# Performance work log

Hardware: AMD Instinct MI355X
Metric: run time of the kernel (lower is better)

The kernel has to match this reference:

```python
import jax, jax.numpy as jnp
import numpy as np

# Static problem sizes (uniform T/taus make the ragged edge list static).
B, N, F, T, TAU, S = 8, 384, 64, 192, 192, 5
SINK_SHIFT = T                    # min sink index == T (sinks are the new nodes)
N_SINK, N_SOURCE = TAU, T + TAU - 1


def _edge_indices():
    # tril_indices(T+tau, offset=-1), keep sink >= T  (window=None)
    r, c = np.tril_indices(T + TAU, k=-1)
    m = r >= T
    r, c = r[m], c[m]
    e = r.shape[0]
    batch = np.repeat(np.arange(B), e)
    return (jnp.asarray(batch, jnp.int32),
            jnp.asarray(np.tile(r, B), jnp.int32),
            jnp.asarray(np.tile(c, B), jnp.int32))


def setup_inputs() -> dict:
    key = jax.random.key(0)
    ks = jax.random.split(key, 6)
    batch_idx, sink_idx, source_idx = _edge_indices()
    s1, s2 = 1.0 / np.sqrt(2 * F), 1.0 / np.sqrt(F)
    return {
        "nodes": jax.random.normal(ks[0], (B, N, F), jnp.float32),
        "w1": jax.random.uniform(ks[1], (2 * F, F), jnp.float32, -s1, s1),
        "b1": jnp.zeros((F,), jnp.float32),
        "g1": jnp.ones((F,), jnp.float32),
        "be1": jnp.zeros((F,), jnp.float32),
        "w2": jax.random.uniform(ks[2], (F, F), jnp.float32, -s2, s2),
        "b2": jnp.zeros((F,), jnp.float32),
        "g2": jnp.ones((F,), jnp.float32),
        "be2": jnp.zeros((F,), jnp.float32),
        "w3": jax.random.uniform(ks[3], (F, 1), jnp.float32, -s2, s2),
        "b3": jnp.zeros((1,), jnp.float32),
        "gumbel": jax.random.gumbel(ks[4], (S, B, N_SINK, N_SOURCE), jnp.float32),
        "batch_idx": batch_idx,
        "sink_idx": sink_idx,
        "source_idx": source_idx,
    }


def _ln(x, g, b):
    mu = x.mean(-1, keepdims=True)
    v = ((x - mu) ** 2).mean(-1, keepdims=True)
    return (x - mu) * jax.lax.rsqrt(v + 1e-5) * g + b


def reference(nodes, w1, b1, g1, be1, w2, b2, g2, be2, w3, b3,
              gumbel, batch_idx, sink_idx, source_idx):
    # gather sink/source node pairs: [E, 2F]
    sink = nodes[batch_idx, sink_idx]
    src = nodes[batch_idx, source_idx]
    x = jnp.concatenate([sink, src], axis=-1)
    # edge MLP -> per-edge logit
    h = _ln(jax.nn.relu(x @ w1 + b1), g1, be1)
    h = _ln(jax.nn.relu(h @ w2 + b2), g2, be2)
    logits = (h @ w3 + b3)[:, 0]                     # [E]
    # dense-padded grid filled with finfo.min (as in torch)
    neg = jnp.finfo(jnp.float32).min
    gs = jnp.full((B, N_SINK, N_SOURCE), neg, jnp.float32)
    gs = gs.at[batch_idx, sink_idx - SINK_SHIFT, source_idx].set(logits)
    # hard gumbel-softmax over source dim, S independent samples
    y_soft = jax.nn.softmax(gs[None] + gumbel, axis=-1)      # [S,B,192,383]
    y_hard = jax.nn.one_hot(jnp.argmax(y_soft, -1), N_SOURCE, dtype=y_soft.dtype)
    y = y_soft + jax.lax.stop_gradient(y_hard - y_soft)
    e = y.sum(0)
    # straight-through binarize: forward (e>0), backward identity
    e = e + jax.lax.stop_gradient((e > 0).astype(e.dtype) - e)
    valid = e[batch_idx, sink_idx - SINK_SHIFT, source_idx]
    vals = jnp.where(valid > 0, valid, 0.0)
    # dense equivalent of the sparse COO adjacency (B, N, N)
    return jnp.zeros((B, N, N), jnp.float32).at[batch_idx, sink_idx, source_idx].set(vals)
```

## Files before the change

kernel.cpp:

```cpp
#include <hip/hip_runtime.h>
#include <math.h>
#include <stdint.h>

#define BB 8
#define NN 384
#define FF 64
#define TT 192
#define NSRC 383
#define NSINK 192
#define SS 5
#define NEDGE 441600
#define BN (BB * NN)
#define TILE_E 256
#define NBLKE (NEDGE / TILE_E)
#define OUTV ((BB * NN * NN) / 4)

typedef _Float16 half8 __attribute__((ext_vector_type(8)));
typedef __fp16 fp16x2 __attribute__((ext_vector_type(2)));
typedef float floatx4 __attribute__((ext_vector_type(4)));

static __device__ __forceinline__ void split_f16(float x, uint16_t& h, uint16_t& l) {
  const _Float16 hh = (_Float16)x;
  const float hb = (float)hh;
  const _Float16 ll = (_Float16)((x - hb) * 512.f);
  h = __builtin_bit_cast(uint16_t, hh);
  l = __builtin_bit_cast(uint16_t, ll);
}

static __device__ __forceinline__ void split_pair(float x0, float x1,
                                                  uint32_t& hi, uint32_t& lo) {
  const fp16x2 h = __builtin_amdgcn_cvt_pkrtz(x0, x1);
  const float hb0 = (float)h.x, hb1 = (float)h.y;
  const fp16x2 l = __builtin_amdgcn_cvt_pkrtz((x0 - hb0) * 512.f, (x1 - hb1) * 512.f);
  hi = __builtin_bit_cast(uint32_t, h);
  lo = __builtin_bit_cast(uint32_t, l);
}

__global__ __launch_bounds__(64) void prep_all(
    const float* __restrict__ nodes, const float* __restrict__ w1,
    const float* __restrict__ b1,
    const float* __restrict__ w2, const float* __restrict__ b2,
    const float* __restrict__ g1, const float* __restrict__ be1,
    const float* __restrict__ g2, const float* __restrict__ be2,
    const float* __restrict__ w3, const float* __restrict__ b3,
    float* __restrict__ A, float* __restrict__ Bv,
    unsigned short* __restrict__ Whg, unsigned short* __restrict__ Wlg,
    float* __restrict__ wcol, float* __restrict__ cb,
    float* __restrict__ gw, float* __restrict__ cwsgw) {
  const int blk = blockIdx.x;
  const int k = threadIdx.x;
  if (blk < BN / 4) {
    const int bn0 = blk * 4;
    __shared__ float nd[4][FF];
#pragma unroll
    for (int i = 0; i < 4; ++i) nd[i][k] = nodes[(bn0 + i) * FF + k];
    __syncthreads();
    const float bk = b1[k];
    float a0 = bk, a1 = bk, a2 = bk, a3 = bk;
    float q0 = 0.f, q1 = 0.f, q2 = 0.f, q3 = 0.f;
#pragma unroll 8
    for (int f = 0; f < FF; ++f) {
      const float wt = w1[f * FF + k];
      const float wb = w1[(FF + f) * FF + k];
      const float n0 = nd[0][f], n1 = nd[1][f], n2 = nd[2][f], n3 = nd[3][f];
      a0 = fmaf(n0, wt, a0); a1 = fmaf(n1, wt, a1);
      a2 = fmaf(n2, wt, a2); a3 = fmaf(n3, wt, a3);
      q0 = fmaf(n0, wb, q0); q1 = fmaf(n1, wb, q1);
      q2 = fmaf(n2, wb, q2); q3 = fmaf(n3, wb, q3);
    }
    A[(bn0 + 0) * FF + k] = a0;  Bv[(bn0 + 0) * FF + k] = q0;
    A[(bn0 + 1) * FF + k] = a1;  Bv[(bn0 + 1) * FF + k] = q1;
    A[(bn0 + 2) * FF + k] = a2;  Bv[(bn0 + 2) * FF + k] = q2;
    A[(bn0 + 3) * FF + k] = a3;  Bv[(bn0 + 3) * FF + k] = q3;
  } else {
    const int j = k;
    const int jt = j >> 4, m = j & 15;
    float cbj = b2[j];
    float wc = 0.f;
    for (int kk = 0; kk < FF; ++kk) {
      const float wraw = w2[kk * FF + j];
      const float w = g1[kk] * wraw;
      wc += w;
      cbj = fmaf(be1[kk], wraw, cbj);
      uint16_t hu, lu;
      split_f16(w, hu, lu);
      const int kc = kk >> 5, qq = (kk >> 3) & 3, jj = kk & 7;
      const int idx = (((jt * 2 + kc) * 4 + qq) * 16 + m) * 8 + jj;
      Whg[idx] = hu;
      Wlg[idx] = lu;
    }
    wcol[j] = wc;
    cb[j] = cbj;
    const float gwj = g2[j] * w3[j];
    gw[j] = gwj;
    __shared__ float sA[FF], sB[FF];
    sA[j] = gwj;
    sB[j] = be2[j] * w3[j];
    __syncthreads();
    if (j == 0) {
      float a = 0.f, bq = 0.f;
      for (int i = 0; i < FF; ++i) { a += sA[i]; bq += sB[i]; }
      cwsgw[0] = b3[0] + bq;
      cwsgw[1] = a;
    }
  }
}

__global__ __launch_bounds__(256, 2) void edge_mlp(
    const float* __restrict__ A, const float* __restrict__ Bv,
    const unsigned short* __restrict__ Whg, const unsigned short* __restrict__ Wlg,
    const float* __restrict__ wcolg, const float* __restrict__ cbg,
    const float* __restrict__ gwg, const float* __restrict__ cwsgw,
    const int* __restrict__ bidx, const int* __restrict__ ridx,
    const int* __restrict__ cidx, float* __restrict__ L,
    float4* __restrict__ outv) {
  __shared__ __align__(16) unsigned short XHs[16384];
  __shared__ __align__(16) unsigned short XLs[16384];

  const int tid = threadIdx.x;
  const int wave = tid >> 6;
  const int lane = tid & 63;
  const int q4 = lane >> 4;
  const int c15 = lane & 15;

  const int gtid = blockIdx.x * 256 + tid;
  if (gtid < OUTV) outv[gtid] = make_float4(0.f, 0.f, 0.f, 0.f);

  half8 whr[4][2], wlr[4][2];
#pragma unroll
  for (int jt = 0; jt < 4; ++jt)
#pragma unroll
    for (int kc = 0; kc < 2; ++kc) {
      const int woff = ((jt * 2 + kc) * 4 + q4) * 128 + c15 * 8;
      whr[jt][kc] = *(const half8*)&Whg[woff];
      wlr[jt][kc] = *(const half8*)&Wlg[woff];
    }

  const int ge = blockIdx.x * TILE_E + tid;
  const int b = bidx[ge], r = ridx[ge], c = cidx[ge];
  const int et_own = lane >> 4, n_own = lane & 15;
  float mu, rstd;
  {
    const float4* pa = (const float4*)(A + (b * NN + r) * FF);
    const float4* pb = (const float4*)(Bv + (b * NN + c) * FF);
    unsigned short* dh = &XHs[wave * 4096 + n_own * 8];
    unsigned short* dl = &XLs[wave * 4096 + n_own * 8];
    float s = 0.f, q = 0.f;
#pragma unroll
    for (int g = 0; g < 8; ++g) {
      const float4 av0 = pa[2 * g], av1 = pa[2 * g + 1];
      const float4 bv0 = pb[2 * g], bv1 = pb[2 * g + 1];
      const float x0 = fmaxf(av0.x + bv0.x, 0.f);
      const float x1 = fmaxf(av0.y + bv0.y, 0.f);
      const float x2 = fmaxf(av0.z + bv0.z, 0.f);
      const float x3 = fmaxf(av0.w + bv0.w, 0.f);
      const float x4 = fmaxf(av1.x + bv1.x, 0.f);
      const float x5 = fmaxf(av1.y + bv1.y, 0.f);
      const float x6 = fmaxf(av1.z + bv1.z, 0.f);
      const float x7 = fmaxf(av1.w + bv1.w, 0.f);
      s += x0 + x1 + x2 + x3 + x4 + x5 + x6 + x7;
      q = fmaf(x0, x0, q); q = fmaf(x1, x1, q);
      q = fmaf(x2, x2, q); q = fmaf(x3, x3, q);
      q = fmaf(x4, x4, q); q = fmaf(x5, x5, q);
      q = fmaf(x6, x6, q); q = fmaf(x7, x7, q);
      int4 hi4, lo4;
      split_pair(x0, x1, *(uint32_t*)&hi4.x, *(uint32_t*)&lo4.x);
      split_pair(x2, x3, *(uint32_t*)&hi4.y, *(uint32_t*)&lo4.y);
      split_pair(x4, x5, *(uint32_t*)&hi4.z, *(uint32_t*)&lo4.z);
      split_pair(x6, x7, *(uint32_t*)&hi4.w, *(uint32_t*)&lo4.w);
      const int choff = ((et_own * 2 + (g >> 2)) * 4 + (g & 3)) * 128;
      *(int4*)(dh + choff) = hi4;
      *(int4*)(dl + choff) = lo4;
    }
    mu = s * (1.f / FF);
    rstd = 1.f / sqrtf(q * (1.f / FF) - mu * mu + 1e-5f);
  }

  __syncthreads();

  floatx4 wc4[4], cb4[4], gw4[4];
#pragma unroll
  for (int jt = 0; jt < 4; ++jt) {
    wc4[jt] = *(const floatx4*)(wcolg + 16 * jt + 4 * q4);
    cb4[jt] = *(const floatx4*)(cbg + 16 * jt + 4 * q4);
    gw4[jt] = *(const floatx4*)(gwg + 16 * jt + 4 * q4);
  }
  const float cw = cwsgw[0], sgw = cwsgw[1];

#pragma unroll
  for (int et = 0; et < 4; ++et) {
    floatx4 acc0[4], acc1[4];
#pragma unroll
    for (int jt = 0; jt < 4; ++jt) {
      acc0[jt] = (floatx4){0.f, 0.f, 0.f, 0.f};
      acc1[jt] = (floatx4){0.f, 0.f, 0.f, 0.f};
    }
#pragma unroll
    for (int kc = 0; kc < 2; ++kc) {
      const int xoff = wave * 4096 + ((et * 2 + kc) * 4 + q4) * 128 + c15 * 8;
      const half8 xh = *(const half8*)&XHs[xoff];
      const half8 xl = *(const half8*)&XLs[xoff];
#pragma unroll
      for (int jt = 0; jt < 4; ++jt) {
        acc0[jt] = __builtin_amdgcn_mfma_f32_16x16x32_f16(whr[jt][kc], xh, acc0[jt], 0, 0, 0);
        acc1[jt] = __builtin_amdgcn_mfma_f32_16x16x32_f16(whr[jt][kc], xl, acc1[jt], 0, 0, 0);
        acc1[jt] = __builtin_amdgcn_mfma_f32_16x16x32_f16(wlr[jt][kc], xh, acc1[jt], 0, 0, 0);
      }
    }
    const int e2 = 16 * et + c15;
    const float mue = __shfl(mu, e2, 64);
    const float rse = __shfl(rstd, e2, 64);
    float s1 = 0.f, s2 = 0.f, s3 = 0.f;
#pragma unroll
    for (int jt = 0; jt < 4; ++jt) {
      const floatx4 t4 = acc0[jt] + acc1[jt] * (1.f / 512.f);
#pragma unroll
      for (int rg = 0; rg < 4; ++rg) {
        const float pre = fmaf(rse, fmaf(-mue, wc4[jt][rg], t4[rg]), cb4[jt][rg]);
        const float tr = fmaxf(pre, 0.f);
        s1 += tr;
        s2 = fmaf(tr, tr, s2);
        s3 = fmaf(tr, gw4[jt][rg], s3);
      }
    }
    s1 += __shfl_xor(s1, 16, 64); s1 += __shfl_xor(s1, 32, 64);
    s2 += __shfl_xor(s2, 16, 64); s2 += __shfl_xor(s2, 32, 64);
    s3 += __shfl_xor(s3, 16, 64); s3 += __shfl_xor(s3, 32, 64);
    const int b2 = __shfl(b, e2, 64);
    const int r2 = __shfl(r, e2, 64);
    const int c2 = __shfl(c, e2, 64);
    if (q4 == 0) {
      const float mu2 = s1 * (1.f / FF);
      const float var2 = s2 * (1.f / FF) - mu2 * mu2;
      const float rstd2 = 1.f / sqrtf(var2 + 1e-5f);
      const float logit = fmaf(rstd2, fmaf(-mu2, sgw, s3), cw);
      L[(b2 * NSINK + (r2 - TT)) * NSRC + c2] = logit;
    }
  }
}

__global__ __launch_bounds__(256) void argmax_scatter(
    const float* __restrict__ L, const float* __restrict__ gum,
    float* __restrict__ out) {
  const int task = blockIdx.x * 4 + (threadIdx.x >> 6);
  const int lane = threadIdx.x & 63;
  const int row = task % NSINK;
  const int sb = task / NSINK;
  const int b = sb & 7;
  const int r = row + TT;

  const float* __restrict__ lrow = L + (b * NSINK + row) * NSRC;
  const float* __restrict__ grow = gum + task * NSRC;

  float bv = -INFINITY;
  int bi = 0;
  for (int c = lane; c < r; c += 64) {
    const float v = lrow[c] + grow[c];
    if (v > bv) { bv = v; bi = c; }
  }
#pragma unroll
  for (int off = 32; off > 0; off >>= 1) {
    const float ov = __shfl_xor(bv, off, 64);
    const int oi = __shfl_xor(bi, off, 64);
    if (ov > bv || (ov == bv && oi < bi)) { bv = ov; bi = oi; }
  }
  if (lane == 0) out[(b * NN + r) * NN + bi] = 1.0f;
}

extern "C" void kernel_launch(void* const* d_in, const int* in_sizes, int n_in,
                              void* d_out, int out_size, void* d_ws, size_t ws_size,
                              hipStream_t stream) {
  const float* nodes = (const float*)d_in[0];
  const float* w1 = (const float*)d_in[1];
  const float* b1 = (const float*)d_in[2];
  const float* g1 = (const float*)d_in[3];
  const float* be1 = (const float*)d_in[4];
  const float* w2 = (const float*)d_in[5];
  const float* b2 = (const float*)d_in[6];
  const float* g2 = (const float*)d_in[7];
  const float* be2 = (const float*)d_in[8];
  const float* w3 = (const float*)d_in[9];
  const float* b3 = (const float*)d_in[10];
  const float* gum = (const float*)d_in[11];
  const int* bidx = (const int*)d_in[12];
  const int* ridx = (const int*)d_in[13];
  const int* cidx = (const int*)d_in[14];
  float* out = (float*)d_out;

  float* ws = (float*)d_ws;
  float* A = ws;
  float* Bv = A + BN * FF;
  unsigned short* Whg = (unsigned short*)(ws + 393216);
  unsigned short* Wlg = Whg + 4096;
  float* wcol = ws + 397312;
  float* cb = wcol + FF;
  float* gw = cb + FF;
  float* cwsgw = gw + FF;
  float* L = ws + 397520;
  (void)ws_size; (void)n_in; (void)in_sizes; (void)out_size;

  hipLaunchKernelGGL(prep_all, dim3(BN / 4 + 1), dim3(64), 0, stream,
                     nodes, w1, b1, w2, b2, g1, be1, g2, be2, w3, b3,
                     A, Bv, Whg, Wlg, wcol, cb, gw, cwsgw);
  hipLaunchKernelGGL(edge_mlp, dim3(NBLKE), dim3(256), 0, stream,
                     A, Bv, Whg, Wlg, wcol, cb, gw, cwsgw, bidx, ridx, cidx, L,
                     (float4*)out);
  hipLaunchKernelGGL(argmax_scatter, dim3((SS * BB * NSINK) / 4), dim3(256), 0, stream,
                     L, gum, out);
}
```

Before: 134.7 us.

## Shrink edge MLP blocks, center inputs before split, drop block barrier

Halves the edge tile and block size to 128 threads with new launch bounds, so LDS per block shrinks and more blocks can be resident. Replaces __syncthreads with a wave barrier, since each wave only reads its own LDS region. Computes the layer-1 mean in a first pass and subtracts it before the f16 hi/lo split, which removes the wcol correction term and its loads. The cost is reading the A and B rows twice per edge.

```diff
diff --git a/kernel.cpp b/kernel.cpp
--- a/kernel.cpp
+++ b/kernel.cpp
@@ -11,7 +11,7 @@
 #define SS 5
 #define NEDGE 441600
 #define BN (BB * NN)
-#define TILE_E 256
+#define TILE_E 128
 #define NBLKE (NEDGE / TILE_E)
 #define OUTV ((BB * NN * NN) / 4)
 
@@ -45,8 +45,7 @@
     const float* __restrict__ w3, const float* __restrict__ b3,
     float* __restrict__ A, float* __restrict__ Bv,
     unsigned short* __restrict__ Whg, unsigned short* __restrict__ Wlg,
-    float* __restrict__ wcol, float* __restrict__ cb,
-    float* __restrict__ gw, float* __restrict__ cwsgw) {
+    float* __restrict__ cb, float* __restrict__ gw, float* __restrict__ cwsgw) {
   const int blk = blockIdx.x;
   const int k = threadIdx.x;
   if (blk < BN / 4) {
@@ -76,11 +75,9 @@
     const int j = k;
     const int jt = j >> 4, m = j & 15;
     float cbj = b2[j];
-    float wc = 0.f;
     for (int kk = 0; kk < FF; ++kk) {
       const float wraw = w2[kk * FF + j];
       const float w = g1[kk] * wraw;
-      wc += w;
       cbj = fmaf(be1[kk], wraw, cbj);
       uint16_t hu, lu;
       split_f16(w, hu, lu);
@@ -89,7 +86,6 @@
       Whg[idx] = hu;
       Wlg[idx] = lu;
     }
-    wcol[j] = wc;
     cb[j] = cbj;
     const float gwj = g2[j] * w3[j];
     gw[j] = gwj;
@@ -106,16 +102,16 @@
   }
 }
 
-__global__ __launch_bounds__(256, 2) void edge_mlp(
+__global__ __launch_bounds__(128, 3) void edge_mlp(
     const float* __restrict__ A, const float* __restrict__ Bv,
     const unsigned short* __restrict__ Whg, const unsigned short* __restrict__ Wlg,
-    const float* __restrict__ wcolg, const float* __restrict__ cbg,
-    const float* __restrict__ gwg, const float* __restrict__ cwsgw,
+    const float* __restrict__ cbg, const float* __restrict__ gwg,
+    const float* __restrict__ cwsgw,
     const int* __restrict__ bidx, const int* __restrict__ ridx,
     const int* __restrict__ cidx, float* __restrict__ L,
     float4* __restrict__ outv) {
-  __shared__ __align__(16) unsigned short XHs[16384];
-  __shared__ __align__(16) unsigned short XLs[16384];
+  __shared__ __align__(16) unsigned short XHs[8192];
+  __shared__ __align__(16) unsigned short XLs[8192];
 
   const int tid = threadIdx.x;
   const int wave = tid >> 6;
@@ -123,46 +119,47 @@
   const int q4 = lane >> 4;
   const int c15 = lane & 15;
 
-  const int gtid = blockIdx.x * 256 + tid;
+  const int gtid = blockIdx.x * 128 + tid;
   if (gtid < OUTV) outv[gtid] = make_float4(0.f, 0.f, 0.f, 0.f);
-
-  half8 whr[4][2], wlr[4][2];
-#pragma unroll
-  for (int jt = 0; jt < 4; ++jt)
-#pragma unroll
-    for (int kc = 0; kc < 2; ++kc) {
-      const int woff = ((jt * 2 + kc) * 4 + q4) * 128 + c15 * 8;
-      whr[jt][kc] = *(const half8*)&Whg[woff];
-      wlr[jt][kc] = *(const half8*)&Wlg[woff];
-    }
 
   const int ge = blockIdx.x * TILE_E + tid;
   const int b = bidx[ge], r = ridx[ge], c = cidx[ge];
   const int et_own = lane >> 4, n_own = lane & 15;
+  const float4* pa = (const float4*)(A + (b * NN + r) * FF);
+  const float4* pb = (const float4*)(Bv + (b * NN + c) * FF);
   float mu, rstd;
   {
-    const float4* pa = (const float4*)(A + (b * NN + r) * FF);
-    const float4* pb = (const float4*)(Bv + (b * NN + c) * FF);
+    float s = 0.f, q = 0.f;
+#pragma unroll
+    for (int i = 0; i < 16; ++i) {
+      const float4 av = pa[i];
+      const float4 bv = pb[i];
+      const float x0 = fmaxf(av.x + bv.x, 0.f);
+      const float x1 = fmaxf(av.y + bv.y, 0.f);
+      const float x2 = fmaxf(av.z + bv.z, 0.f);
+      const float x3 = fmaxf(av.w + bv.w, 0.f);
+      s += x0 + x1 + x2 + x3;
+      q = fmaf(x0, x0, q); q = fmaf(x1, x1, q);
+      q = fmaf(x2, x2, q); q = fmaf(x3, x3, q);
+    }
+    mu = s * (1.f / FF);
+    rstd = 1.f / sqrtf(q * (1.f / FF) - mu * mu + 1e-5f);
+  }
+  {
     unsigned short* dh = &XHs[wave * 4096 + n_own * 8];
     unsigned short* dl = &XLs[wave * 4096 + n_own * 8];
-    float s = 0.f, q = 0.f;
 #pragma unroll
     for (int g = 0; g < 8; ++g) {
       const float4 av0 = pa[2 * g], av1 = pa[2 * g + 1];
       const float4 bv0 = pb[2 * g], bv1 = pb[2 * g + 1];
-      const float x0 = fmaxf(av0.x + bv0.x, 0.f);
-      const float x1 = fmaxf(av0.y + bv0.y, 0.f);
-      const float x2 = fmaxf(av0.z + bv0.z, 0.f);
-      const float x3 = fmaxf(av0.w + bv0.w, 0.f);
-      const float x4 = fmaxf(av1.x + bv1.x, 0.f);
-      const float x5 = fmaxf(av1.y + bv1.y, 0.f);
-      const float x6 = fmaxf(av1.z + bv1.z, 0.f);
-      const float x7 = fmaxf(av1.w + bv1.w, 0.f);
-      s += x0 + x1 + x2 + x3 + x4 + x5 + x6 + x7;
-      q = fmaf(x0, x0, q); q = fmaf(x1, x1, q);
-      q = fmaf(x2, x2, q); q = fmaf(x3, x3, q);
-      q = fmaf(x4, x4, q); q = fmaf(x5, x5, q);
-      q = fmaf(x6, x6, q); q = fmaf(x7, x7, q);
+      const float x0 = fmaxf(av0.x + bv0.x, 0.f) - mu;
+      const float x1 = fmaxf(av0.y + bv0.y, 0.f) - mu;
+      const float x2 = fmaxf(av0.z + bv0.z, 0.f) - mu;
+      const float x3 = fmaxf(av0.w + bv0.w, 0.f) - mu;
+      const float x4 = fmaxf(av1.x + bv1.x, 0.f) - mu;
+      const float x5 = fmaxf(av1.y + bv1.y, 0.f) - mu;
+      const float x6 = fmaxf(av1.z + bv1.z, 0.f) - mu;
+      const float x7 = fmaxf(av1.w + bv1.w, 0.f) - mu;
       int4 hi4, lo4;
       split_pair(x0, x1, *(uint32_t*)&hi4.x, *(uint32_t*)&lo4.x);
       split_pair(x2, x3, *(uint32_t*)&hi4.y, *(uint32_t*)&lo4.y);
@@ -172,16 +169,23 @@
       *(int4*)(dh + choff) = hi4;
       *(int4*)(dl + choff) = lo4;
     }
-    mu = s * (1.f / FF);
-    rstd = 1.f / sqrtf(q * (1.f / FF) - mu * mu + 1e-5f);
-  }
-
-  __syncthreads();
-
-  floatx4 wc4[4], cb4[4], gw4[4];
+  }
+
+  half8 whr[4][2], wlr[4][2];
+#pragma unroll
+  for (int jt = 0; jt < 4; ++jt)
+#pragma unroll
+    for (int kc = 0; kc < 2; ++kc) {
+      const int woff = ((jt * 2 + kc) * 4 + q4) * 128 + c15 * 8;
+      whr[jt][kc] = *(const half8*)&Whg[woff];
+      wlr[jt][kc] = *(const half8*)&Wlg[woff];
+    }
+
+  __builtin_amdgcn_wave_barrier();
+
+  floatx4 cb4[4], gw4[4];
 #pragma unroll
   for (int jt = 0; jt < 4; ++jt) {
-    wc4[jt] = *(const floatx4*)(wcolg + 16 * jt + 4 * q4);
     cb4[jt] = *(const floatx4*)(cbg + 16 * jt + 4 * q4);
     gw4[jt] = *(const floatx4*)(gwg + 16 * jt + 4 * q4);
   }
@@ -208,7 +212,6 @@
       }
     }
     const int e2 = 16 * et + c15;
-    const float mue = __shfl(mu, e2, 64);
     const float rse = __shfl(rstd, e2, 64);
     float s1 = 0.f, s2 = 0.f, s3 = 0.f;
 #pragma unroll
@@ -216,7 +219,7 @@
       const floatx4 t4 = acc0[jt] + acc1[jt] * (1.f / 512.f);
 #pragma unroll
       for (int rg = 0; rg < 4; ++rg) {
-        const float pre = fmaf(rse, fmaf(-mue, wc4[jt][rg], t4[rg]), cb4[jt][rg]);
+        const float pre = fmaf(rse, t4[rg], cb4[jt][rg]);
         const float tr = fmaxf(pre, 0.f);
         s1 += tr;
         s2 = fmaf(tr, tr, s2);
@@ -292,8 +295,7 @@
   float* Bv = A + BN * FF;
   unsigned short* Whg = (unsigned short*)(ws + 393216);
   unsigned short* Wlg = Whg + 4096;
-  float* wcol = ws + 397312;
-  float* cb = wcol + FF;
+  float* cb = ws + 397312;
   float* gw = cb + FF;
   float* cwsgw = gw + FF;
   float* L = ws + 397520;
@@ -301,9 +303,9 @@
 
   hipLaunchKernelGGL(prep_all, dim3(BN / 4 + 1), dim3(64), 0, stream,
                      nodes, w1, b1, w2, b2, g1, be1, g2, be2, w3, b3,
-                     A, Bv, Whg, Wlg, wcol, cb, gw, cwsgw);
-  hipLaunchKernelGGL(edge_mlp, dim3(NBLKE), dim3(256), 0, stream,
-                     A, Bv, Whg, Wlg, wcol, cb, gw, cwsgw, bidx, ridx, cidx, L,
+                     A, Bv, Whg, Wlg, cb, gw, cwsgw);
+  hipLaunchKernelGGL(edge_mlp, dim3(NBLKE), dim3(128), 0, stream,
+                     A, Bv, Whg, Wlg, cb, gw, cwsgw, bidx, ridx, cidx, L,
                      (float4*)out);
   hipLaunchKernelGGL(argmax_scatter, dim3((SS * BB * NSINK) / 4), dim3(256), 0, stream,
                      L, gum, out);
```

Result: slower. 214.7 us (+59.4%).
